# Optimization experiments

Hardware: AMD Instinct MI355X
Metric: run time of the kernel (lower is better)

The kernel has to match this reference:

```python
import jax, jax.numpy as jnp
import numpy as np

B, N, F_IN, UNITS, E, MAX_VIEW = 4, 10000, 64, 64, 160000, 3
C = F_IN + UNITS  # concat channel dim (num_embedding)


def setup_inputs() -> dict:
    key = jax.random.key(0)
    ks = jax.random.split(key, 8)
    inputs = jax.random.normal(ks[0], (B, N, F_IN), jnp.float32)
    hx = jax.random.normal(ks[1], (B, N, UNITS), jnp.float32)
    sparse_idx = jax.random.randint(ks[2], (2, E), 0, N)          # row0=src, row1=dst
    conv_ker = jax.random.normal(ks[3], (E,), jnp.float32) * 0.1  # per-edge kernel weight
    W_ru = jax.random.normal(ks[4], (MAX_VIEW * C, 2 * UNITS), jnp.float32) * 0.05
    b_ru = jnp.zeros((2 * UNITS,), jnp.float32)
    W_c = jax.random.normal(ks[5], (MAX_VIEW * C, UNITS), jnp.float32) * 0.05
    b_c = jnp.zeros((UNITS,), jnp.float32)
    return dict(inputs=inputs, hx=hx, sparse_idx=sparse_idx, conv_ker=conv_ker,
                W_ru=W_ru, b_ru=b_ru, W_c=W_c, b_c=b_c)


def _graph_conv(x, src, dst, ker, W, b):
    """Multi-view sparse graph conv: [x, A x, A^2 x, ...] concat -> linear.
    x: (B, N, C); edge e aggregates ker[e] * x[:, src[e]] into node dst[e]."""
    views = [x]
    y = x
    for _ in range(MAX_VIEW - 1):
        msg = y[:, src, :] * ker[None, :, None]        # (B, E, C) gather + scale
        y = jnp.zeros_like(x).at[:, dst, :].add(msg)   # (B, N, C) scatter-add
        views.append(y)
    h = jnp.concatenate(views, axis=-1)                # (B, N, MAX_VIEW*C)
    return h @ W + b


def reference(inputs, hx, sparse_idx, conv_ker, W_ru, b_ru, W_c, b_c):
    src, dst = sparse_idx[0], sparse_idx[1]
    # GRU r,u gates from graph conv over concat(inputs, hx)
    x_ru = jnp.concatenate([inputs, hx], axis=-1)                      # (B, N, C)
    ru = jax.nn.sigmoid(_graph_conv(x_ru, src, dst, conv_ker, W_ru, b_ru))
    r, u = jnp.split(ru, 2, axis=-1)                                   # (B, N, UNITS) each
    # candidate state from graph conv over concat(inputs, r*hx)
    x_c = jnp.concatenate([inputs, r * hx], axis=-1)
    c = jnp.tanh(_graph_conv(x_c, src, dst, conv_ker, W_c, b_c))
    return u * hx + (1.0 - u) * c
```

## Files before the change

### kernel.cpp

```cpp
#include <hip/hip_runtime.h>
#include <hip/hip_bf16.h>
#include <math.h>

#define NB 10000
#define BB 4
#define CC 128
#define EE 160000
#define MM (NB * BB)

typedef __attribute__((ext_vector_type(8))) short short8;
typedef __attribute__((ext_vector_type(4))) float floatx4;

struct ViewTab {
  const ushort* base[12];
  int stride[12];
};


__device__ inline unsigned pk(float a, float b) {
  __hip_bfloat16 ha = __float2bfloat16(a), hb = __float2bfloat16(b);
  unsigned short ua = *(unsigned short*)&ha, ub = *(unsigned short*)&hb;
  return (unsigned)ua | ((unsigned)ub << 16);
}

__device__ inline void fma8(float* a, uint4 v, float k) {
  a[0] += k * __uint_as_float(v.x << 16);
  a[1] += k * __uint_as_float(v.x & 0xffff0000u);
  a[2] += k * __uint_as_float(v.y << 16);
  a[3] += k * __uint_as_float(v.y & 0xffff0000u);
  a[4] += k * __uint_as_float(v.z << 16);
  a[5] += k * __uint_as_float(v.z & 0xffff0000u);
  a[6] += k * __uint_as_float(v.w << 16);
  a[7] += k * __uint_as_float(v.w & 0xffff0000u);
}


__global__ void k_count(const int* __restrict__ dst, int* __restrict__ cnt) {
  int e = blockIdx.x * blockDim.x + threadIdx.x;
  if (e < EE) atomicAdd(&cnt[dst[e]], 1);
}

__global__ __launch_bounds__(1024) void k_scan(const int* __restrict__ cnt,
                                               int* __restrict__ off,
                                               int* __restrict__ cur) {
  __shared__ int s_cnt[10240];
  __shared__ int s_sum[1024];
  int t = threadIdx.x;
  for (int i = t; i < 10240; i += 1024) s_cnt[i] = (i < NB) ? cnt[i] : 0;
  __syncthreads();
  int base = t * 10;
  int acc = 0;
  int loc[10];
#pragma unroll
  for (int i = 0; i < 10; ++i) { loc[i] = acc; acc += s_cnt[base + i]; }
  s_sum[t] = acc;
  __syncthreads();
  for (int d = 1; d < 1024; d <<= 1) {
    int v = (t >= d) ? s_sum[t - d] : 0;
    __syncthreads();
    s_sum[t] += v;
    __syncthreads();
  }
  int prev = (t == 0) ? 0 : s_sum[t - 1];
#pragma unroll
  for (int i = 0; i < 10; ++i) {
    int idx = base + i;
    int val = prev + loc[i];
    if (idx <= NB) off[idx] = val;
    if (idx < NB) cur[idx] = val;
  }
}

__global__ void k_fill(const int* __restrict__ src, const int* __restrict__ dst,
                       const float* __restrict__ ker, int* __restrict__ cur,
                       uint2* __restrict__ edges) {
  int e = blockIdx.x * blockDim.x + threadIdx.x;
  if (e < EE) {
    int p = atomicAdd(&cur[dst[e]], 1);
    edges[p] = make_uint2((unsigned)src[e], __float_as_uint(ker[e]));
  }
}


__global__ void k_convW(const float* __restrict__ Wru, const float* __restrict__ Wc,
                        ushort* __restrict__ Wtru, ushort* __restrict__ Wtc) {
  int t = blockIdx.x * blockDim.x + threadIdx.x;
  if (t < 128 * 384) {
    int nn = t / 384, kk = t % 384;
    __hip_bfloat16 h = __float2bfloat16(Wru[(size_t)kk * 128 + nn]);
    Wtru[t] = *(unsigned short*)&h;
  }
  if (t < 64 * 384) {
    int nn = t / 384, kk = t % 384;
    __hip_bfloat16 h = __float2bfloat16(Wc[(size_t)kk * 64 + nn]);
    Wtc[t] = *(unsigned short*)&h;
  }
}


__global__ void k_build_xru(const float* __restrict__ in, const float* __restrict__ hx,
                            ushort* __restrict__ x) {
  int tid = blockIdx.x * blockDim.x + threadIdx.x;
  int m = tid >> 4;
  int c8 = (tid & 15) << 3;
  int n = m >> 2, b = m & 3;
  const float* sp = (c8 < 64) ? (in + (size_t)(b * NB + n) * 64 + c8)
                              : (hx + (size_t)(b * NB + n) * 64 + (c8 - 64));
  float4 f0 = *(const float4*)(sp);
  float4 f1 = *(const float4*)(sp + 4);
  uint4 o;
  o.x = pk(f0.x, f0.y); o.y = pk(f0.z, f0.w);
  o.z = pk(f1.x, f1.y); o.w = pk(f1.z, f1.w);
  *(uint4*)(x + (size_t)m * 128 + c8) = o;
}

__global__ void k_build_rh(const float* __restrict__ ru, const float* __restrict__ hx,
                           ushort* __restrict__ rh) {
  int tid = blockIdx.x * blockDim.x + threadIdx.x;
  int m = tid >> 3;
  int c8 = (tid & 7) << 3;
  int n = m >> 2, b = m & 3;
  const float* rp = ru + (size_t)m * 128 + c8;
  const float* hp = hx + (size_t)(b * NB + n) * 64 + c8;
  float4 r0 = *(const float4*)rp, r1 = *(const float4*)(rp + 4);
  float4 h0 = *(const float4*)hp, h1 = *(const float4*)(hp + 4);
  uint4 o;
  o.x = pk(r0.x * h0.x, r0.y * h0.y);
  o.y = pk(r0.z * h0.z, r0.w * h0.w);
  o.z = pk(r1.x * h1.x, r1.y * h1.y);
  o.w = pk(r1.z * h1.z, r1.w * h1.w);
  *(uint4*)(rh + (size_t)m * 64 + c8) = o;
}


__global__ __launch_bounds__(256) void k_prop(const ushort* __restrict__ x,
                                              ushort* __restrict__ y,
                                              const int* __restrict__ roff,
                                              const uint2* __restrict__ edges) {
  int tid = blockIdx.x * blockDim.x + threadIdx.x;
  int n = tid >> 6;
  int o8 = (tid & 63) << 3;
  int beg = roff[n], end = roff[n + 1];
  float acc[8];
#pragma unroll
  for (int j = 0; j < 8; ++j) acc[j] = 0.f;
  int i = beg;
  for (; i + 2 <= end; i += 2) {
    uint2 e0 = edges[i], e1 = edges[i + 1];
    uint4 v0 = *(const uint4*)(x + (size_t)e0.x * 512 + o8);
    uint4 v1 = *(const uint4*)(x + (size_t)e1.x * 512 + o8);
    fma8(acc, v0, __uint_as_float(e0.y));
    fma8(acc, v1, __uint_as_float(e1.y));
  }
  if (i < end) {
    uint2 e0 = edges[i];
    uint4 v0 = *(const uint4*)(x + (size_t)e0.x * 512 + o8);
    fma8(acc, v0, __uint_as_float(e0.y));
  }
  uint4 o;
  o.x = pk(acc[0], acc[1]); o.y = pk(acc[2], acc[3]);
  o.z = pk(acc[4], acc[5]); o.w = pk(acc[6], acc[7]);
  *(uint4*)(y + (size_t)n * 512 + o8) = o;
}

__global__ __launch_bounds__(256) void k_prop64(const ushort* __restrict__ x,
                                                ushort* __restrict__ y,
                                                const int* __restrict__ roff,
                                                const uint2* __restrict__ edges) {
  int tid = blockIdx.x * blockDim.x + threadIdx.x;
  int n = tid >> 5;
  int o8 = (tid & 31) << 3;
  int beg = roff[n], end = roff[n + 1];
  float acc[8];
#pragma unroll
  for (int j = 0; j < 8; ++j) acc[j] = 0.f;
  int i = beg;
  for (; i + 2 <= end; i += 2) {
    uint2 e0 = edges[i], e1 = edges[i + 1];
    uint4 v0 = *(const uint4*)(x + (size_t)e0.x * 256 + o8);
    uint4 v1 = *(const uint4*)(x + (size_t)e1.x * 256 + o8);
    fma8(acc, v0, __uint_as_float(e0.y));
    fma8(acc, v1, __uint_as_float(e1.y));
  }
  if (i < end) {
    uint2 e0 = edges[i];
    uint4 v0 = *(const uint4*)(x + (size_t)e0.x * 256 + o8);
    fma8(acc, v0, __uint_as_float(e0.y));
  }
  uint4 o;
  o.x = pk(acc[0], acc[1]); o.y = pk(acc[2], acc[3]);
  o.z = pk(acc[4], acc[5]); o.w = pk(acc[6], acc[7]);
  *(uint4*)(y + (size_t)n * 256 + o8) = o;
}


template <int NT, bool FINAL>
__global__ __launch_bounds__(256) void k_gemm_mfma(
    ViewTab V, const ushort* __restrict__ Wt,
    const float* __restrict__ bias, float* __restrict__ ru,
    const float* __restrict__ hx, float* __restrict__ out) {
  const int tid = threadIdx.x;
  const int lane = tid & 63;
  const int w = tid >> 6;
  const int wm = w >> 1, wn = w & 1;
  const int m0 = blockIdx.x * 64 + wm * 32;
  const int col0 = wn * (NT * 16);
  const int lr = lane & 15;
  const int quad = lane >> 4;
  const int koff = quad * 8;

  floatx4 acc[2][NT];
#pragma unroll
  for (int a = 0; a < 2; ++a)
#pragma unroll
    for (int b = 0; b < NT; ++b) acc[a][b] = {0.f, 0.f, 0.f, 0.f};

#pragma unroll
  for (int kt = 0; kt < 12; ++kt) {
    const ushort* bp = V.base[kt];
    const int st = V.stride[kt];
    const int kg = (kt << 5) + koff;
    short8 a0 = *(const short8*)(bp + (size_t)(m0 + lr) * st + koff);
    short8 a1 = *(const short8*)(bp + (size_t)(m0 + 16 + lr) * st + koff);
#pragma unroll
    for (int nt = 0; nt < NT; ++nt) {
      short8 b = *(const short8*)(Wt + (size_t)(col0 + nt * 16 + lr) * 384 + kg);
      acc[0][nt] = __builtin_amdgcn_mfma_f32_16x16x32_bf16(a0, b, acc[0][nt], 0, 0, 0);
      acc[1][nt] = __builtin_amdgcn_mfma_f32_16x16x32_bf16(a1, b, acc[1][nt], 0, 0, 0);
    }
  }

#pragma unroll
  for (int mt = 0; mt < 2; ++mt) {
#pragma unroll
    for (int nt = 0; nt < NT; ++nt) {
      int col = col0 + nt * 16 + lr;
      float bv = bias[col];
#pragma unroll
      for (int i = 0; i < 4; ++i) {
        int m = m0 + mt * 16 + quad * 4 + i;
        float val = acc[mt][nt][i] + bv;
        if (!FINAL) {
          ru[(size_t)m * 128 + col] = 1.f / (1.f + expf(-val));
        } else {
          int n = m >> 2, b2 = m & 3;
          float u = ru[(size_t)m * 128 + 64 + col];
          float h = hx[(size_t)(b2 * NB + n) * 64 + col];
          float c = tanhf(val);
          out[(size_t)(b2 * NB + n) * 64 + col] = u * h + (1.f - u) * c;
        }
      }
    }
  }
}


extern "C" void kernel_launch(void* const* d_in, const int* in_sizes, int n_in,
                              void* d_out, int out_size, void* d_ws, size_t ws_size,
                              hipStream_t stream) {
  const float* d_inputs = (const float*)d_in[0];
  const float* d_hx     = (const float*)d_in[1];
  const int*   d_sidx   = (const int*)d_in[2];
  const float* d_ker    = (const float*)d_in[3];
  const float* d_Wru    = (const float*)d_in[4];
  const float* d_bru    = (const float*)d_in[5];
  const float* d_Wc     = (const float*)d_in[6];
  const float* d_bc     = (const float*)d_in[7];
  float* out = (float*)d_out;
  const int* src = d_sidx;
  const int* dst = d_sidx + EE;

  ushort* x    = (ushort*)d_ws;
  ushort* y1   = x + (size_t)MM * 128;
  ushort* y2   = y1 + (size_t)MM * 128;
  ushort* rh0  = y2 + (size_t)MM * 128;
  ushort* rh1  = rh0 + (size_t)MM * 64;
  ushort* rh2  = rh1 + (size_t)MM * 64;
  float*  ru   = (float*)(rh2 + (size_t)MM * 64);
  ushort* Wtru = (ushort*)(ru + (size_t)MM * 128);
  ushort* Wtc  = Wtru + 128 * 384;
  uint2*  edges = (uint2*)(Wtc + 64 * 384);
  int*    cnt  = (int*)(edges + EE);
  int*    off  = cnt + NB;
  int*    cur  = off + NB + 1;

  hipMemsetAsync(cnt, 0, NB * sizeof(int), stream);
  k_count<<<(EE + 255) / 256, 256, 0, stream>>>(dst, cnt);
  k_scan<<<1, 1024, 0, stream>>>(cnt, off, cur);
  k_fill<<<(EE + 255) / 256, 256, 0, stream>>>(src, dst, d_ker, cur, edges);
  k_convW<<<(128 * 384 + 255) / 256, 256, 0, stream>>>(d_Wru, d_Wc, Wtru, Wtc);

  k_build_xru<<<(MM * 16) / 256, 256, 0, stream>>>(d_inputs, d_hx, x);
  k_prop<<<(NB * 64) / 256, 256, 0, stream>>>(x, y1, off, edges);
  k_prop<<<(NB * 64) / 256, 256, 0, stream>>>(y1, y2, off, edges);
  ViewTab V1;
  for (int t = 0; t < 12; ++t) {
    const ushort* ten = (t < 4) ? x : (t < 8) ? y1 : y2;
    V1.base[t] = ten + (t & 3) * 32;
    V1.stride[t] = 128;
  }
  k_gemm_mfma<4, false><<<MM / 64, 256, 0, stream>>>(V1, Wtru, d_bru, ru, nullptr, nullptr);

  k_build_rh<<<(MM * 8) / 256, 256, 0, stream>>>(ru, d_hx, rh0);
  k_prop64<<<(NB * 32) / 256, 256, 0, stream>>>(rh0, rh1, off, edges);
  k_prop64<<<(NB * 32) / 256, 256, 0, stream>>>(rh1, rh2, off, edges);
  ViewTab V2;
  {
    const ushort* c1[3] = {x, y1, y2};
    const ushort* c2[3] = {rh0, rh1, rh2};
    for (int v = 0; v < 3; ++v) {
      V2.base[v * 4 + 0] = c1[v];      V2.stride[v * 4 + 0] = 128;
      V2.base[v * 4 + 1] = c1[v] + 32; V2.stride[v * 4 + 1] = 128;
      V2.base[v * 4 + 2] = c2[v];      V2.stride[v * 4 + 2] = 64;
      V2.base[v * 4 + 3] = c2[v] + 32; V2.stride[v * 4 + 3] = 64;
    }
  }
  k_gemm_mfma<2, true><<<MM / 64, 256, 0, stream>>>(V2, Wtc, d_bc, ru, d_hx, out);
}
```

Measured before the change: 247.4 us.

## Switch to batch-major layout, split edges across lanes, fuse r*hx into gate GEMM

Switches the activation layout from node-interleaved (n*4+b) to batch-major (b*N+n), so input and hx reads become contiguous. The propagation kernels now give each wavefront one (batch, node) pair, spread its edges across lane groups, and combine the partial sums with cross-lane shuffles. The gate GEMM epilogue now writes r*hx and u directly as bf16, which removes the separate build_rh kernel and the fp32 ru buffer. Each GEMM block now handles two row tiles. The costs are shuffle reductions, idle lanes on nodes with few edges, and extra rounding of u to bf16.

```diff
diff --git a/kernel.cpp b/kernel.cpp
--- a/kernel.cpp
+++ b/kernel.cpp
@@ -4,7 +4,6 @@
 
 #define NB 10000
 #define BB 4
-#define CC 128
 #define EE 160000
 #define MM (NB * BB)
 
@@ -21,6 +20,11 @@
   __hip_bfloat16 ha = __float2bfloat16(a), hb = __float2bfloat16(b);
   unsigned short ua = *(unsigned short*)&ha, ub = *(unsigned short*)&hb;
   return (unsigned)ua | ((unsigned)ub << 16);
+}
+
+__device__ inline float bf2f(ushort u) {
+  unsigned v = (unsigned)u << 16;
+  return __uint_as_float(v);
 }
 
 __device__ inline void fma8(float* a, uint4 v, float k) {
@@ -103,9 +107,8 @@
   int tid = blockIdx.x * blockDim.x + threadIdx.x;
   int m = tid >> 4;
   int c8 = (tid & 15) << 3;
-  int n = m >> 2, b = m & 3;
-  const float* sp = (c8 < 64) ? (in + (size_t)(b * NB + n) * 64 + c8)
-                              : (hx + (size_t)(b * NB + n) * 64 + (c8 - 64));
+  const float* sp = (c8 < 64) ? (in + (size_t)m * 64 + c8)
+                              : (hx + (size_t)m * 64 + (c8 - 64));
   float4 f0 = *(const float4*)(sp);
   float4 f1 = *(const float4*)(sp + 4);
   uint4 o;
@@ -114,140 +117,161 @@
   *(uint4*)(x + (size_t)m * 128 + c8) = o;
 }
 
-__global__ void k_build_rh(const float* __restrict__ ru, const float* __restrict__ hx,
-                           ushort* __restrict__ rh) {
-  int tid = blockIdx.x * blockDim.x + threadIdx.x;
-  int m = tid >> 3;
-  int c8 = (tid & 7) << 3;
-  int n = m >> 2, b = m & 3;
-  const float* rp = ru + (size_t)m * 128 + c8;
-  const float* hp = hx + (size_t)(b * NB + n) * 64 + c8;
-  float4 r0 = *(const float4*)rp, r1 = *(const float4*)(rp + 4);
-  float4 h0 = *(const float4*)hp, h1 = *(const float4*)(hp + 4);
-  uint4 o;
-  o.x = pk(r0.x * h0.x, r0.y * h0.y);
-  o.y = pk(r0.z * h0.z, r0.w * h0.w);
-  o.z = pk(r1.x * h1.x, r1.y * h1.y);
-  o.w = pk(r1.z * h1.z, r1.w * h1.w);
-  *(uint4*)(rh + (size_t)m * 64 + c8) = o;
-}
-
-
-__global__ __launch_bounds__(256) void k_prop(const ushort* __restrict__ x,
-                                              ushort* __restrict__ y,
-                                              const int* __restrict__ roff,
-                                              const uint2* __restrict__ edges) {
-  int tid = blockIdx.x * blockDim.x + threadIdx.x;
-  int n = tid >> 6;
-  int o8 = (tid & 63) << 3;
+
+__global__ __launch_bounds__(256) void k_prop128(const ushort* __restrict__ x,
+                                                 ushort* __restrict__ y,
+                                                 const int* __restrict__ roff,
+                                                 const uint2* __restrict__ edges) {
+  int blk = blockIdx.x;
+  int b = (blk & 7) >> 1;
+  int jb = ((blk >> 3) << 1) | (blk & 1);
+  int w = threadIdx.x >> 6;
+  int lane = threadIdx.x & 63;
+  int n = jb * 4 + w;
+  int g = lane >> 4;
+  int o8 = (lane & 15) << 3;
+  const ushort* xb = x + (size_t)b * NB * 128;
   int beg = roff[n], end = roff[n + 1];
   float acc[8];
 #pragma unroll
   for (int j = 0; j < 8; ++j) acc[j] = 0.f;
-  int i = beg;
-  for (; i + 2 <= end; i += 2) {
-    uint2 e0 = edges[i], e1 = edges[i + 1];
-    uint4 v0 = *(const uint4*)(x + (size_t)e0.x * 512 + o8);
-    uint4 v1 = *(const uint4*)(x + (size_t)e1.x * 512 + o8);
+  int i = beg + g;
+  for (; i + 4 < end; i += 8) {
+    uint2 e0 = edges[i], e1 = edges[i + 4];
+    uint4 v0 = *(const uint4*)(xb + (size_t)e0.x * 128 + o8);
+    uint4 v1 = *(const uint4*)(xb + (size_t)e1.x * 128 + o8);
     fma8(acc, v0, __uint_as_float(e0.y));
     fma8(acc, v1, __uint_as_float(e1.y));
   }
   if (i < end) {
     uint2 e0 = edges[i];
-    uint4 v0 = *(const uint4*)(x + (size_t)e0.x * 512 + o8);
+    uint4 v0 = *(const uint4*)(xb + (size_t)e0.x * 128 + o8);
     fma8(acc, v0, __uint_as_float(e0.y));
   }
-  uint4 o;
-  o.x = pk(acc[0], acc[1]); o.y = pk(acc[2], acc[3]);
-  o.z = pk(acc[4], acc[5]); o.w = pk(acc[6], acc[7]);
-  *(uint4*)(y + (size_t)n * 512 + o8) = o;
+#pragma unroll
+  for (int j = 0; j < 8; ++j) {
+    acc[j] += __shfl_xor(acc[j], 16);
+    acc[j] += __shfl_xor(acc[j], 32);
+  }
+  if (g == 0) {
+    uint4 o;
+    o.x = pk(acc[0], acc[1]); o.y = pk(acc[2], acc[3]);
+    o.z = pk(acc[4], acc[5]); o.w = pk(acc[6], acc[7]);
+    *(uint4*)(y + (size_t)b * NB * 128 + (size_t)n * 128 + o8) = o;
+  }
 }
 
 __global__ __launch_bounds__(256) void k_prop64(const ushort* __restrict__ x,
                                                 ushort* __restrict__ y,
                                                 const int* __restrict__ roff,
                                                 const uint2* __restrict__ edges) {
-  int tid = blockIdx.x * blockDim.x + threadIdx.x;
-  int n = tid >> 5;
-  int o8 = (tid & 31) << 3;
+  int blk = blockIdx.x;
+  int b = (blk & 7) >> 1;
+  int jb = ((blk >> 3) << 1) | (blk & 1);
+  int w = threadIdx.x >> 6;
+  int lane = threadIdx.x & 63;
+  int n = jb * 4 + w;
+  int g = lane >> 3;
+  int o8 = (lane & 7) << 3;
+  const ushort* xb = x + (size_t)b * NB * 64;
   int beg = roff[n], end = roff[n + 1];
   float acc[8];
 #pragma unroll
   for (int j = 0; j < 8; ++j) acc[j] = 0.f;
-  int i = beg;
-  for (; i + 2 <= end; i += 2) {
-    uint2 e0 = edges[i], e1 = edges[i + 1];
-    uint4 v0 = *(const uint4*)(x + (size_t)e0.x * 256 + o8);
-    uint4 v1 = *(const uint4*)(x + (size_t)e1.x * 256 + o8);
+  int i = beg + g;
+  for (; i + 8 < end; i += 16) {
+    uint2 e0 = edges[i], e1 = edges[i + 8];
+    uint4 v0 = *(const uint4*)(xb + (size_t)e0.x * 64 + o8);
+    uint4 v1 = *(const uint4*)(xb + (size_t)e1.x * 64 + o8);
     fma8(acc, v0, __uint_as_float(e0.y));
     fma8(acc, v1, __uint_as_float(e1.y));
   }
   if (i < end) {
     uint2 e0 = edges[i];
-    uint4 v0 = *(const uint4*)(x + (size_t)e0.x * 256 + o8);
+    uint4 v0 = *(const uint4*)(xb + (size_t)e0.x * 64 + o8);
     fma8(acc, v0, __uint_as_float(e0.y));
   }
-  uint4 o;
-  o.x = pk(acc[0], acc[1]); o.y = pk(acc[2], acc[3]);
-  o.z = pk(acc[4], acc[5]); o.w = pk(acc[6], acc[7]);
-  *(uint4*)(y + (size_t)n * 256 + o8) = o;
-}
-
-
-template <int NT, bool FINAL>
+#pragma unroll
+  for (int j = 0; j < 8; ++j) {
+    acc[j] += __shfl_xor(acc[j], 8);
+    acc[j] += __shfl_xor(acc[j], 16);
+    acc[j] += __shfl_xor(acc[j], 32);
+  }
+  if (g == 0) {
+    uint4 o;
+    o.x = pk(acc[0], acc[1]); o.y = pk(acc[2], acc[3]);
+    o.z = pk(acc[4], acc[5]); o.w = pk(acc[6], acc[7]);
+    *(uint4*)(y + (size_t)b * NB * 64 + (size_t)n * 64 + o8) = o;
+  }
+}
+
+
+template <int NT, int MREP, bool FINAL>
 __global__ __launch_bounds__(256) void k_gemm_mfma(
-    ViewTab V, const ushort* __restrict__ Wt,
-    const float* __restrict__ bias, float* __restrict__ ru,
-    const float* __restrict__ hx, float* __restrict__ out) {
+    ViewTab V, const ushort* __restrict__ Wt, const float* __restrict__ bias,
+    ushort* __restrict__ rh0, ushort* __restrict__ u,
+    const ushort* __restrict__ uu, const float* __restrict__ hx,
+    float* __restrict__ out) {
   const int tid = threadIdx.x;
   const int lane = tid & 63;
   const int w = tid >> 6;
   const int wm = w >> 1, wn = w & 1;
-  const int m0 = blockIdx.x * 64 + wm * 32;
   const int col0 = wn * (NT * 16);
   const int lr = lane & 15;
   const int quad = lane >> 4;
   const int koff = quad * 8;
 
-  floatx4 acc[2][NT];
-#pragma unroll
-  for (int a = 0; a < 2; ++a)
-#pragma unroll
-    for (int b = 0; b < NT; ++b) acc[a][b] = {0.f, 0.f, 0.f, 0.f};
-
-#pragma unroll
-  for (int kt = 0; kt < 12; ++kt) {
-    const ushort* bp = V.base[kt];
-    const int st = V.stride[kt];
-    const int kg = (kt << 5) + koff;
-    short8 a0 = *(const short8*)(bp + (size_t)(m0 + lr) * st + koff);
-    short8 a1 = *(const short8*)(bp + (size_t)(m0 + 16 + lr) * st + koff);
-#pragma unroll
-    for (int nt = 0; nt < NT; ++nt) {
-      short8 b = *(const short8*)(Wt + (size_t)(col0 + nt * 16 + lr) * 384 + kg);
-      acc[0][nt] = __builtin_amdgcn_mfma_f32_16x16x32_bf16(a0, b, acc[0][nt], 0, 0, 0);
-      acc[1][nt] = __builtin_amdgcn_mfma_f32_16x16x32_bf16(a1, b, acc[1][nt], 0, 0, 0);
+  for (int rep = 0; rep < MREP; ++rep) {
+    const int m0 = (blockIdx.x * MREP + rep) * 64 + wm * 32;
+    if (m0 >= MM) break;
+
+    floatx4 acc[2][NT];
+#pragma unroll
+    for (int a = 0; a < 2; ++a)
+#pragma unroll
+      for (int b = 0; b < NT; ++b) acc[a][b] = {0.f, 0.f, 0.f, 0.f};
+
+#pragma unroll
+    for (int kt = 0; kt < 12; ++kt) {
+      const ushort* bp = V.base[kt];
+      const int st = V.stride[kt];
+      const int kg = (kt << 5) + koff;
+      short8 a0 = *(const short8*)(bp + (size_t)(m0 + lr) * st + koff);
+      short8 a1 = *(const short8*)(bp + (size_t)(m0 + 16 + lr) * st + koff);
+#pragma unroll
+      for (int nt = 0; nt < NT; ++nt) {
+        short8 b = *(const short8*)(Wt + (size_t)(col0 + nt * 16 + lr) * 384 + kg);
+        acc[0][nt] = __builtin_amdgcn_mfma_f32_16x16x32_bf16(a0, b, acc[0][nt], 0, 0, 0);
+        acc[1][nt] = __builtin_amdgcn_mfma_f32_16x16x32_bf16(a1, b, acc[1][nt], 0, 0, 0);
+      }
     }
-  }
-
-#pragma unroll
-  for (int mt = 0; mt < 2; ++mt) {
-#pragma unroll
-    for (int nt = 0; nt < NT; ++nt) {
-      int col = col0 + nt * 16 + lr;
-      float bv = bias[col];
-#pragma unroll
-      for (int i = 0; i < 4; ++i) {
-        int m = m0 + mt * 16 + quad * 4 + i;
-        float val = acc[mt][nt][i] + bv;
-        if (!FINAL) {
-          ru[(size_t)m * 128 + col] = 1.f / (1.f + expf(-val));
-        } else {
-          int n = m >> 2, b2 = m & 3;
-          float u = ru[(size_t)m * 128 + 64 + col];
-          float h = hx[(size_t)(b2 * NB + n) * 64 + col];
-          float c = tanhf(val);
-          out[(size_t)(b2 * NB + n) * 64 + col] = u * h + (1.f - u) * c;
+
+#pragma unroll
+    for (int mt = 0; mt < 2; ++mt) {
+#pragma unroll
+      for (int nt = 0; nt < NT; ++nt) {
+        int col = col0 + nt * 16 + lr;
+        float bv = bias[col];
+#pragma unroll
+        for (int i = 0; i < 4; ++i) {
+          int m = m0 + mt * 16 + quad * 4 + i;
+          float val = acc[mt][nt][i] + bv;
+          if (!FINAL) {
+            float s = 1.f / (1.f + expf(-val));
+            if (col < 64) {
+              float r = s * hx[(size_t)m * 64 + col];
+              __hip_bfloat16 hb = __float2bfloat16(r);
+              rh0[(size_t)m * 64 + col] = *(unsigned short*)&hb;
+            } else {
+              __hip_bfloat16 hb = __float2bfloat16(s);
+              u[(size_t)m * 64 + (col - 64)] = *(unsigned short*)&hb;
+            }
+          } else {
+            float uv = bf2f(uu[(size_t)m * 64 + col]);
+            float h = hx[(size_t)m * 64 + col];
+            float c = tanhf(val);
+            out[(size_t)m * 64 + col] = uv * h + (1.f - uv) * c;
+          }
         }
       }
     }
@@ -276,8 +300,8 @@
   ushort* rh0  = y2 + (size_t)MM * 128;
   ushort* rh1  = rh0 + (size_t)MM * 64;
   ushort* rh2  = rh1 + (size_t)MM * 64;
-  float*  ru   = (float*)(rh2 + (size_t)MM * 64);
-  ushort* Wtru = (ushort*)(ru + (size_t)MM * 128);
+  ushort* u    = rh2 + (size_t)MM * 64;
+  ushort* Wtru = u + (size_t)MM * 64;
   ushort* Wtc  = Wtru + 128 * 384;
   uint2*  edges = (uint2*)(Wtc + 64 * 384);
   int*    cnt  = (int*)(edges + EE);
@@ -291,19 +315,19 @@
   k_convW<<<(128 * 384 + 255) / 256, 256, 0, stream>>>(d_Wru, d_Wc, Wtru, Wtc);
 
   k_build_xru<<<(MM * 16) / 256, 256, 0, stream>>>(d_inputs, d_hx, x);
-  k_prop<<<(NB * 64) / 256, 256, 0, stream>>>(x, y1, off, edges);
-  k_prop<<<(NB * 64) / 256, 256, 0, stream>>>(y1, y2, off, edges);
+  k_prop128<<<10000, 256, 0, stream>>>(x, y1, off, edges);
+  k_prop128<<<10000, 256, 0, stream>>>(y1, y2, off, edges);
   ViewTab V1;
   for (int t = 0; t < 12; ++t) {
     const ushort* ten = (t < 4) ? x : (t < 8) ? y1 : y2;
     V1.base[t] = ten + (t & 3) * 32;
     V1.stride[t] = 128;
   }
-  k_gemm_mfma<4, false><<<MM / 64, 256, 0, stream>>>(V1, Wtru, d_bru, ru, nullptr, nullptr);
-
-  k_build_rh<<<(MM * 8) / 256, 256, 0, stream>>>(ru, d_hx, rh0);
-  k_prop64<<<(NB * 32) / 256, 256, 0, stream>>>(rh0, rh1, off, edges);
-  k_prop64<<<(NB * 32) / 256, 256, 0, stream>>>(rh1, rh2, off, edges);
+  k_gemm_mfma<4, 2, false><<<313, 256, 0, stream>>>(V1, Wtru, d_bru, rh0, u,
+                                                    nullptr, d_hx, nullptr);
+
+  k_prop64<<<10000, 256, 0, stream>>>(rh0, rh1, off, edges);
+  k_prop64<<<10000, 256, 0, stream>>>(rh1, rh2, off, edges);
   ViewTab V2;
   {
     const ushort* c1[3] = {x, y1, y2};
@@ -315,5 +339,6 @@
       V2.base[v * 4 + 3] = c2[v] + 32; V2.stride[v * 4 + 3] = 64;
     }
   }
-  k_gemm_mfma<2, true><<<MM / 64, 256, 0, stream>>>(V2, Wtc, d_bc, ru, d_hx, out);
-}
+  k_gemm_mfma<2, 2, true><<<313, 256, 0, stream>>>(V2, Wtc, d_bc, nullptr, nullptr,
+                                                   u, d_hx, out);
+}
```

New measurement: 272.0 us. 1.1x slower.
